# Performance work log

Hardware: AMD Instinct MI355X
Metric: run time of the kernel (lower is better)

## Reference

```python
import jax, jax.numpy as jnp
from jax import lax
import numpy as np


def fourier_kernel(coef, xs):
    """Evaluate the real Fourier kernel. coef: (n, idim, odim); xs: (...,).
    Returns (..., idim, odim). Matches torch version: complex exp split into cos/sin,
    interior modes doubled."""
    n = coef.shape[0]
    mh = n // 2 + 1
    rr = coef[:mh]                                   # cosine coeffs (mh, i, o)
    ii = jnp.zeros_like(rr).at[1:n - mh + 1].set(jnp.flip(coef[mh:], axis=0))
    k = 2.0 * jnp.pi * jnp.arange(mh, dtype=xs.dtype)
    ang = k * xs[..., None]                          # (..., mh)
    scale = jnp.ones((mh,), dtype=xs.dtype).at[1:-1].set(2.0)
    cr = jnp.cos(ang) * scale
    si = jnp.sin(ang) * scale
    return jnp.tensordot(cr, rr, 1) - jnp.tensordot(si, ii, 1)


def sem_conv(nodal, coef, ws, grid, ndim, dim):
    """Windowed spectral-element convolution along direction `dim`.
    nodal: (m_0..m_{ndim-1}, E_0..E_{ndim-1}, idim); ws: (s+1, m, m); grid: (m,)."""
    ns = ''.join(chr(120 + i) for i in range(ndim))          # node axes: 'xy'
    o = ns[dim].upper()
    ms = ns.replace(ns[dim], o)
    es = ''.join(chr(97 + i) for i in range(ndim))           # element axes: 'ab'
    eqn = f'{ns}{es}i,{o}{ns[dim]}io,{o}{ns[dim]}->{ms}{es}o'
    ax = ndim + dim                                          # element axis for `dim`
    E = nodal.shape[ax]
    s1 = ws.shape[0]
    r = s1 // 2
    # circular padding along element axis (matches [pad_l, nodal, pad_r])
    pad_l = lax.slice_in_dim(nodal, E - r, E, axis=ax)
    pad_r = lax.slice_in_dim(nodal, 0, r, axis=ax)
    f = jnp.concatenate([pad_l, nodal, pad_r], axis=ax)
    out = None
    for k in range(s1):                                      # small fixed window loop
        xy = (grid[:, None] - (grid[None, :] + (k - r))) / (s1 - 1)   # (m, m)
        g = fourier_kernel(coef, xy)                         # (m, m, idim, odim)
        fx = lax.slice_in_dim(f, k, k + E, axis=ax)
        term = jnp.einsum(eqn, fx, g, ws[k])
        out = term if out is None else out + term
    return out


def setup_inputs() -> dict:
    key = jax.random.key(0)
    k1, k2, k3, k4, k5 = jax.random.split(key, 5)
    m, E, idim, odim, mode, s = 8, 144, 16, 16, 16, 4
    nodal = jax.random.normal(k1, (m, m, E, E, idim), dtype=jnp.float32)
    coef0 = jax.random.normal(k2, (s * mode, idim, odim), dtype=jnp.float32) * 0.02
    coef1 = jax.random.normal(k3, (s * mode, idim, odim), dtype=jnp.float32) * 0.02
    ws0 = jax.random.normal(k4, (s + 1, m, m), dtype=jnp.float32) * 0.1
    ws1 = jax.random.normal(k5, (s + 1, m, m), dtype=jnp.float32) * 0.1
    grid = jnp.linspace(0.0, 1.0, m, dtype=jnp.float32)
    return {"nodal": nodal, "coef0": coef0, "coef1": coef1,
            "ws0": ws0, "ws1": ws1, "grid": grid}


def reference(nodal, coef0, coef1, ws0, ws1, grid):
    # SEMConv.__call__: sum of factorized convolutions over each spatial dim
    return (sem_conv(nodal, coef0, ws0, grid, 2, 0)
            + sem_conv(nodal, coef1, ws1, grid, 2, 1))
```

## Files before the change

### kernel.cpp

```cpp
#include <hip/hip_runtime.h>

typedef __attribute__((ext_vector_type(8))) short short8;
typedef __attribute__((ext_vector_type(4))) float f32x4;

#define NODAL_ELEMS 21233664
#define BSLAB 81920
#define NB_OFF 327680
#define C0_OFF (NB_OFF + (size_t)NODAL_ELEMS * 2)

__device__ __forceinline__ unsigned short f2bf(float f) {
    unsigned int u = __float_as_uint(f);
    u += 0x7FFFu + ((u >> 16) & 1u);
    return (unsigned short)(u >> 16);
}
__device__ __forceinline__ float bf2f(unsigned short s) {
    return __uint_as_float(((unsigned int)s) << 16);
}

__device__ __forceinline__ void gload_lds16(const void* g, void* l) {
    __builtin_amdgcn_global_load_lds(
        (const __attribute__((address_space(1))) unsigned int*)g,
        (__attribute__((address_space(3))) unsigned int*)l, 16, 0, 0);
}

__global__ void build_b_kernel(const float* __restrict__ coef0,
                               const float* __restrict__ coef1,
                               const float* __restrict__ ws0,
                               const float* __restrict__ ws1,
                               const float* __restrict__ grid,
                               unsigned short* __restrict__ B)
{
    const int bid = blockIdx.x;
    const int d   = (bid >= 320) ? 1 : 0;
    const int rem = bid - d * 320;
    const int k   = rem >> 6;
    const int X   = (rem >> 3) & 7;
    const int x   = rem & 7;

    const float* __restrict__ coef = d ? coef1 : coef0;
    const float* __restrict__ ws   = d ? ws1 : ws0;
    unsigned short* __restrict__ Bd = B + d * BSLAB;

    const float xy = (grid[X] - (grid[x] + (float)(k - 2))) * 0.25f;
    const int t = threadIdx.x;
    const int i = t >> 4;
    const int o = t & 15;

    float acc = 0.f;
    #pragma unroll 1
    for (int j = 0; j < 33; ++j) {
        float ang = 6.283185307179586f * (float)j * xy;
        float c = cosf(ang);
        float s = sinf(ang);
        float sc = (j == 0 || j == 32) ? 1.f : 2.f;
        float rr = coef[j * 256 + t];
        float ii = (j >= 1 && j <= 31) ? coef[(64 - j) * 256 + t] : 0.f;
        acc += sc * (c * rr - s * ii);
    }
    float val = acc * ws[(k * 8 + X) * 8 + x];

    const int kk = k * 16 + x * 2 + (i >> 3);
    const int jj = i & 7;
    const int n  = X * 16 + o;
    Bd[(kk * 128 + n) * 8 + jj] = f2bf(val);
}

__global__ void cvt_kernel(const float* __restrict__ in,
                           unsigned short* __restrict__ out, int n4)
{
    int idx = blockIdx.x * blockDim.x + threadIdx.x;
    int stride = gridDim.x * blockDim.x;
    for (int j = idx; j < n4; j += stride) {
        float4 v = ((const float4*)in)[j];
        ushort4 r;
        r.x = f2bf(v.x); r.y = f2bf(v.y); r.z = f2bf(v.z); r.w = f2bf(v.w);
        ((ushort4*)out)[j] = r;
    }
}

template<int TERM, bool AB16, bool C0B16>
__global__ __launch_bounds__(256, 3)
void conv_mfma(const float* __restrict__ nodalf,
               const unsigned short* __restrict__ nodalb,
               const unsigned short* __restrict__ Bmat,
               unsigned short* __restrict__ c0,
               float* __restrict__ out)
{
    __shared__ __align__(16) char lds[3][16384];

    const int tid = threadIdx.x;
    const int w   = tid >> 6;
    const int l   = tid & 63;
    const int sub = l >> 4;
    const int lr  = l & 15;

    const int bid  = blockIdx.x;
    const int XF   = bid & 7;
    const int rest = bid >> 3;
    const int half = (rest >= 81) ? 1 : 0;
    const int mt   = rest - half * 81;

    const int scal = (TERM == 0) ? XF * 331776 : XF * 2654208;
    const int KSTR = (TERM == 0) ? 2654208 : 331776;

    int base[2][5];
    const int rowbase = mt * 128 + w * 32;
    #pragma unroll
    for (int mf = 0; mf < 2; ++mf) {
        int row = rowbase + mf * 16 + lr;
        int a = row / 72;
        int b = row - a * 72 + half * 72;
        #pragma unroll
        for (int k = 0; k < 5; ++k) {
            int sh = ((TERM == 0) ? a : b) + k - 2;
            if (sh < 0) sh += 144;
            if (sh >= 144) sh -= 144;
            int off = (TERM == 0) ? (sh * 2304 + b * 16) : (a * 2304 + sh * 16);
            base[mf][k] = off + (sub >> 1) * KSTR + (sub & 1) * 8;
        }
    }

    const unsigned short* nb = nodalb + scal;
    const float* nfp = nodalf + scal;
    const char* Bb = (const char*)Bmat;

    f32x4 acc[2][8];
    #pragma unroll
    for (int mf = 0; mf < 2; ++mf)
        #pragma unroll
        for (int nf = 0; nf < 8; ++nf)
            acc[mf][nf] = (f32x4){0.f, 0.f, 0.f, 0.f};

    short8 Ab[3][2][2];
    float4 Af[3][2][2][2];

#define STAGE_B(buf_, c_) do {                                               \
    _Pragma("unroll")                                                        \
    for (int u_ = 0; u_ < 4; ++u_)                                           \
        gload_lds16(Bb + (c_) * 16384 + u_ * 4096 + tid * 16,                \
                    &lds[buf_][u_ * 4096 + tid * 16]);                       \
} while (0)

#define LOAD_A(slot_, c_) do {                                               \
    _Pragma("unroll")                                                        \
    for (int ksp_ = 0; ksp_ < 2; ++ksp_) {                                   \
        const int ks_ = 2 * (c_) + ksp_;                                     \
        _Pragma("unroll")                                                    \
        for (int mf_ = 0; mf_ < 2; ++mf_) {                                  \
            if (AB16) {                                                      \
                Ab[slot_][ksp_][mf_] = *(const short8*)                      \
                    (nb + base[mf_][ks_ >> 2] + (ks_ & 3) * 2 * KSTR);       \
            } else {                                                         \
                const float* s_ = nfp + base[mf_][ks_ >> 2]                  \
                                      + (ks_ & 3) * 2 * KSTR;                \
                Af[slot_][ksp_][mf_][0] = *(const float4*)s_;                \
                Af[slot_][ksp_][mf_][1] = *(const float4*)(s_ + 4);          \
            }                                                                \
        }                                                                    \
    } } while (0)

#define CHUNK_BARRIER(vm_) do {                                              \
    __builtin_amdgcn_sched_barrier(0);                                       \
    asm volatile("s_waitcnt vmcnt(" vm_ ")" ::: "memory");                   \
    __builtin_amdgcn_s_barrier();                                            \
    __builtin_amdgcn_sched_barrier(0);                                       \
} while (0)

    STAGE_B(0, 0);
    STAGE_B(1, 1);
    __builtin_amdgcn_sched_barrier(0);
    LOAD_A(0, 0);
    LOAD_A(1, 1);
    CHUNK_BARRIER("8");

    #pragma unroll
    for (int c = 0; c < 10; ++c) {
        if (c < 8) {
            STAGE_B((c + 2) % 3, c + 2);
            __builtin_amdgcn_sched_barrier(0);
            LOAD_A((c + 2) % 3, c + 2);
            __builtin_amdgcn_sched_barrier(0);
        }

        #pragma unroll
        for (int ksp = 0; ksp < 2; ++ksp) {
            short8 a0, a1;
            if (AB16) {
                a0 = Ab[c % 3][ksp][0];
                a1 = Ab[c % 3][ksp][1];
            } else {
                #pragma unroll
                for (int e = 0; e < 4; ++e) {
                    a0[e]     = (short)f2bf(((const float*)&Af[c % 3][ksp][0][0])[e]);
                    a0[e + 4] = (short)f2bf(((const float*)&Af[c % 3][ksp][0][1])[e]);
                    a1[e]     = (short)f2bf(((const float*)&Af[c % 3][ksp][1][0])[e]);
                    a1[e + 4] = (short)f2bf(((const float*)&Af[c % 3][ksp][1][1])[e]);
                }
            }

            const char* bbase = lds[c % 3] + ksp * 8192 + sub * 2048 + lr * 16;
            __builtin_amdgcn_s_setprio(1);
            #pragma unroll
            for (int nf = 0; nf < 8; ++nf) {
                short8 bf = *(const short8*)(bbase + nf * 256);
                acc[0][nf] = __builtin_amdgcn_mfma_f32_16x16x32_bf16(
                    a0, bf, acc[0][nf], 0, 0, 0);
                acc[1][nf] = __builtin_amdgcn_mfma_f32_16x16x32_bf16(
                    a1, bf, acc[1][nf], 0, 0, 0);
            }
            __builtin_amdgcn_s_setprio(0);
        }

        if (c < 9) {
            if (c >= 8) CHUNK_BARRIER("0");
            else        CHUNK_BARRIER("8");
        }
    }

    #pragma unroll
    for (int mf = 0; mf < 2; ++mf) {
        #pragma unroll
        for (int r = 0; r < 4; ++r) {
            int row = rowbase + mf * 16 + sub * 4 + r;
            int a = row / 72;
            int b = row - a * 72 + half * 72;
            int ab16i = (a * 144 + b) * 16;
            #pragma unroll
            for (int nf = 0; nf < 8; ++nf) {
                int pq = (TERM == 0) ? (nf * 2654208 + XF * 331776)
                                     : (XF * 2654208 + nf * 331776);
                int idx = pq + ab16i + lr;
                float v = acc[mf][nf][r];
                if (TERM == 0) {
                    if (C0B16) c0[idx] = f2bf(v);
                    else       out[idx] = v;
                } else {
                    if (C0B16) out[idx] = v + bf2f(c0[idx]);
                    else       out[idx] += v;
                }
            }
        }
    }
#undef STAGE_B
#undef LOAD_A
#undef CHUNK_BARRIER
}

extern "C" void kernel_launch(void* const* d_in, const int* in_sizes, int n_in,
                              void* d_out, int out_size, void* d_ws, size_t ws_size,
                              hipStream_t stream) {
    const float* nodal = (const float*)d_in[0];
    const float* coef0 = (const float*)d_in[1];
    const float* coef1 = (const float*)d_in[2];
    const float* ws0   = (const float*)d_in[3];
    const float* ws1   = (const float*)d_in[4];
    const float* grid  = (const float*)d_in[5];
    float* outp = (float*)d_out;

    unsigned short* B      = (unsigned short*)d_ws;
    unsigned short* nodalb = (unsigned short*)((char*)d_ws + NB_OFF);
    unsigned short* c0     = (unsigned short*)((char*)d_ws + C0_OFF);
    const bool ab16 = ws_size >= (size_t)NB_OFF + (size_t)NODAL_ELEMS * 2;
    const bool c0b  = ws_size >= C0_OFF + (size_t)NODAL_ELEMS * 2;

    hipLaunchKernelGGL(build_b_kernel, dim3(640), dim3(256), 0, stream,
                       coef0, coef1, ws0, ws1, grid, B);
    if (ab16)
        hipLaunchKernelGGL(cvt_kernel, dim3(2048), dim3(256), 0, stream,
                           nodal, nodalb, NODAL_ELEMS / 4);

    dim3 g(1296);
    if (ab16 && c0b) {
        hipLaunchKernelGGL((conv_mfma<0, true, true>), g, dim3(256), 0, stream,
                           nodal, nodalb, B, c0, outp);
        hipLaunchKernelGGL((conv_mfma<1, true, true>), g, dim3(256), 0, stream,
                           nodal, nodalb, B + BSLAB, c0, outp);
    } else if (ab16) {
        hipLaunchKernelGGL((conv_mfma<0, true, false>), g, dim3(256), 0, stream,
                           nodal, nodalb, B, c0, outp);
        hipLaunchKernelGGL((conv_mfma<1, true, false>), g, dim3(256), 0, stream,
                           nodal, nodalb, B + BSLAB, c0, outp);
    } else {
        hipLaunchKernelGGL((conv_mfma<0, false, false>), g, dim3(256), 0, stream,
                           nodal, nodalb, B, c0, outp);
        hipLaunchKernelGGL((conv_mfma<1, false, false>), g, dim3(256), 0, stream,
                           nodal, nodalb, B + BSLAB, c0, outp);
    }
}
```

Baseline: 119.6 us.

## Store bf16 intermediate in MFMA fragment order and drop setprio

The bf16 intermediate buffer written by the first term is now stored in a per-lane fragment-ordered layout, so each lane writes and later reads 4 contiguous bf16 values as one vector instead of scattered 2-byte accesses. The second term reads it back through the same layout before writing fp32 output in the original layout. The change also removes the s_setprio bracketing around the MFMA loop and relaxes the last chunk barrier's wait count. It relies on both kernels using identical rest/w/l indexing, and the relaxed barrier count could race if the count is wrong.

```diff
diff --git a/kernel.cpp b/kernel.cpp
--- a/kernel.cpp
+++ b/kernel.cpp
@@ -199,7 +199,6 @@
             }
 
             const char* bbase = lds[c % 3] + ksp * 8192 + sub * 2048 + lr * 16;
-            __builtin_amdgcn_s_setprio(1);
             #pragma unroll
             for (int nf = 0; nf < 8; ++nf) {
                 short8 bf = *(const short8*)(bbase + nf * 256);
@@ -208,35 +207,62 @@
                 acc[1][nf] = __builtin_amdgcn_mfma_f32_16x16x32_bf16(
                     a1, bf, acc[1][nf], 0, 0, 0);
             }
-            __builtin_amdgcn_s_setprio(0);
         }
 
         if (c < 9) {
-            if (c >= 8) CHUNK_BARRIER("0");
+            if (c == 8) CHUNK_BARRIER("4");
             else        CHUNK_BARRIER("8");
         }
     }
 
-    #pragma unroll
-    for (int mf = 0; mf < 2; ++mf) {
-        #pragma unroll
-        for (int r = 0; r < 4; ++r) {
-            int row = rowbase + mf * 16 + sub * 4 + r;
-            int a = row / 72;
-            int b = row - a * 72 + half * 72;
-            int ab16i = (a * 144 + b) * 16;
+    if (C0B16) {
+        #pragma unroll
+        for (int mf = 0; mf < 2; ++mf) {
             #pragma unroll
             for (int nf = 0; nf < 8; ++nf) {
-                int pq = (TERM == 0) ? (nf * 2654208 + XF * 331776)
-                                     : (XF * 2654208 + nf * 331776);
-                int idx = pq + ab16i + lr;
-                float v = acc[mf][nf][r];
+                const int P = (TERM == 0) ? nf : XF;
+                const int Q = (TERM == 0) ? XF : nf;
+                unsigned short* cp = c0 +
+                    (((((size_t)rest * 4 + w) * 2 + mf) * 8 + P) * 8 + Q) * 256
+                    + l * 4;
                 if (TERM == 0) {
-                    if (C0B16) c0[idx] = f2bf(v);
-                    else       out[idx] = v;
+                    ushort4 cs;
+                    cs.x = f2bf(acc[mf][nf][0]);
+                    cs.y = f2bf(acc[mf][nf][1]);
+                    cs.z = f2bf(acc[mf][nf][2]);
+                    cs.w = f2bf(acc[mf][nf][3]);
+                    *(ushort4*)cp = cs;
                 } else {
-                    if (C0B16) out[idx] = v + bf2f(c0[idx]);
-                    else       out[idx] += v;
+                    ushort4 cv = *(const ushort4*)cp;
+                    unsigned short ca[4] = {cv.x, cv.y, cv.z, cv.w};
+                    #pragma unroll
+                    for (int r = 0; r < 4; ++r) {
+                        int row = rowbase + mf * 16 + sub * 4 + r;
+                        int a = row / 72;
+                        int b = row - a * 72 + half * 72;
+                        int idx = XF * 2654208 + nf * 331776 +
+                                  (a * 144 + b) * 16 + lr;
+                        out[idx] = acc[mf][nf][r] + bf2f(ca[r]);
+                    }
+                }
+            }
+        }
+    } else {
+        #pragma unroll
+        for (int mf = 0; mf < 2; ++mf) {
+            #pragma unroll
+            for (int r = 0; r < 4; ++r) {
+                int row = rowbase + mf * 16 + sub * 4 + r;
+                int a = row / 72;
+                int b = row - a * 72 + half * 72;
+                int ab16i = (a * 144 + b) * 16;
+                #pragma unroll
+                for (int nf = 0; nf < 8; ++nf) {
+                    int pq = (TERM == 0) ? (nf * 2654208 + XF * 331776)
+                                         : (XF * 2654208 + nf * 331776);
+                    int idx = pq + ab16i + lr;
+                    if (TERM == 0) out[idx] = acc[mf][nf][r];
+                    else           out[idx] += acc[mf][nf][r];
                 }
             }
         }
```

Result: faster. 115.1 us (-3.8%).
